# Optimization experiments

Hardware: AMD Instinct MI355X
Metric: run time of the kernel (lower is better)

## Reference

```python
import jax, jax.numpy as jnp
import numpy as np

NH = 8          # attention heads
NC = 14         # disease classes
K = 10          # aspect queries per class
E = 1024        # vision_dim == text_dim
HID = 512       # hidden_dim = vision_dim // 2
TEMP = 0.1
LN_EPS = 1e-5


def _layernorm(x, g, b):
    m = jnp.mean(x, axis=-1, keepdims=True)
    v = jnp.mean(jnp.square(x - m), axis=-1, keepdims=True)
    return (x - m) * jax.lax.rsqrt(v + LN_EPS) * g + b


def _mha(q, k, v, in_w, in_b, out_w, out_b):
    # nn.MultiheadAttention (batch_first, eval mode => dropout off)
    B, Lq, Emb = q.shape
    Lk = k.shape[1]
    dh = Emb // NH
    wq, wk, wv = jnp.split(in_w, 3, axis=0)
    bq, bk, bv = jnp.split(in_b, 3)
    qh = (q @ wq.T + bq).reshape(B, Lq, NH, dh)
    kh = (k @ wk.T + bk).reshape(B, Lk, NH, dh)
    vh = (v @ wv.T + bv).reshape(B, Lk, NH, dh)
    scale = np.float32(1.0 / np.sqrt(dh))
    scores = jnp.einsum('bqhd,bkhd->bhqk', qh, kh) * scale
    attn = jax.nn.softmax(scores, axis=-1)
    out = jnp.einsum('bhqk,bkhd->bqhd', attn, vh).reshape(B, Lq, Emb)
    out = out @ out_w.T + out_b
    return out, attn.mean(axis=1)  # avg over heads, (B, Lq, Lk)


def _l2norm(x):
    return x / jnp.maximum(jnp.linalg.norm(x, axis=-1, keepdims=True), 1e-12)


def reference(vision_features, text_embeddings, vision_global, aspect_queries,
              ch_in_w, ch_in_b, ch_out_w, ch_out_b, tp_w, tp_b,
              ca_in_w, ca_in_b, ca_out_w, ca_out_b,
              cross_ln_g, cross_ln_b, cross_fc_w, cross_fc_b,
              dir_ln_g, dir_ln_b, dir_w1, dir_b1, dir_w2, dir_b2):
    B, N, _ = vision_features.shape
    # ---- contrastive branch (1-token query / 1-token kv attention) ----
    text_proj = text_embeddings @ tp_w.T + tp_b               # (B, E)
    c_out, _ = _mha(vision_global[:, None, :], text_proj[:, None, :],
                    text_proj[:, None, :], ch_in_w, ch_in_b, ch_out_w, ch_out_b)
    sim = jnp.sum(_l2norm(c_out[:, 0, :]) * _l2norm(text_proj), axis=-1) / TEMP  # (B,)
    contrastive_logits = jnp.broadcast_to(sim[:, None], (B, NC))
    # ---- supervised branch: fused per-class cross-attention (shared K/V) ----
    q = jnp.broadcast_to(aspect_queries.reshape(1, NC * K, E), (B, NC * K, E))
    att_out, attn_w = _mha(q, vision_features, vision_features,
                           ca_in_w, ca_in_b, ca_out_w, ca_out_b)
    attended = att_out.reshape(B, NC, K, E).mean(axis=2)       # (B, NC, E)
    attention_weights = attn_w.reshape(B, NC, K, N)            # (B, NC, K, N)
    # fc_cross: LN + per-class linear row (class j feature -> class j logit)
    h = _layernorm(attended, cross_ln_g, cross_ln_b)
    logits_cross = jnp.einsum('bjd,jd->bj', h, cross_fc_w) + cross_fc_b
    # fc_direct MLP on global feature
    g = _layernorm(vision_global, dir_ln_g, dir_ln_b)
    logits_direct = jax.nn.relu(g @ dir_w1.T + dir_b1) @ dir_w2.T + dir_b2
    supervised_logits = (logits_cross + logits_direct) * 0.5
    final_logits = (supervised_logits + contrastive_logits) * 0.5
    return contrastive_logits, supervised_logits, final_logits, attention_weights


def setup_inputs() -> dict:
    key = jax.random.key(0)
    ks = jax.random.split(key, 16)
    B, N = 64, 576
    w = lambda k, s: (jax.random.normal(k, s, dtype=jnp.float32) * 0.02)
    return {
        'vision_features': jax.random.normal(ks[0], (B, N, E), dtype=jnp.float32),
        'text_embeddings': jax.random.normal(ks[1], (B, E), dtype=jnp.float32),
        'vision_global': jax.random.normal(ks[2], (B, E), dtype=jnp.float32),
        'aspect_queries': jax.random.normal(ks[3], (NC, K, E), dtype=jnp.float32) / np.sqrt(E).astype(np.float32),
        'ch_in_w': w(ks[4], (3 * E, E)), 'ch_in_b': jnp.zeros((3 * E,), jnp.float32),
        'ch_out_w': w(ks[5], (E, E)), 'ch_out_b': jnp.zeros((E,), jnp.float32),
        'tp_w': w(ks[6], (E, E)), 'tp_b': jnp.zeros((E,), jnp.float32),
        'ca_in_w': w(ks[7], (3 * E, E)), 'ca_in_b': jnp.zeros((3 * E,), jnp.float32),
        'ca_out_w': w(ks[8], (E, E)), 'ca_out_b': jnp.zeros((E,), jnp.float32),
        'cross_ln_g': jnp.ones((E,), jnp.float32), 'cross_ln_b': jnp.zeros((E,), jnp.float32),
        'cross_fc_w': w(ks[9], (NC, E)), 'cross_fc_b': jnp.zeros((NC,), jnp.float32),
        'dir_ln_g': jnp.ones((E,), jnp.float32), 'dir_ln_b': jnp.zeros((E,), jnp.float32),
        'dir_w1': w(ks[10], (HID, E)), 'dir_b1': jnp.zeros((HID,), jnp.float32),
        'dir_w2': w(ks[11], (NC, HID)), 'dir_b2': jnp.zeros((NC,), jnp.float32),
    }
```

## Files before the change

### kernel.cpp

```cpp
#include <hip/hip_runtime.h>
#include <cstdio>
#include <cstdint>

using u16 = unsigned short;
typedef __bf16 bf16x8 __attribute__((ext_vector_type(8)));
typedef float f32x4 __attribute__((ext_vector_type(4)));

#define GLOBAL_AS __attribute__((address_space(1)))
#define LDS_AS __attribute__((address_space(3)))

__device__ __forceinline__ float bf2f(u16 h) {
  return __uint_as_float(((unsigned)h) << 16);
}
__device__ __forceinline__ u16 f2bf(float f) {
  unsigned u = __float_as_uint(f);
  u += 0x7FFFu + ((u >> 16) & 1u);
  return (u16)(u >> 16);
}

__device__ __forceinline__ void async_copy16(void* lds, const void* g) {
  __builtin_amdgcn_global_load_lds((const GLOBAL_AS unsigned int*)g,
                                   (LDS_AS unsigned int*)lds, 16, 0, 0);
}

__device__ __forceinline__ float block_sum(float v, float* red) {
#pragma unroll
  for (int o = 32; o >= 1; o >>= 1) v += __shfl_xor(v, o);
  __syncthreads();
  if ((threadIdx.x & 63) == 0) red[threadIdx.x >> 6] = v;
  __syncthreads();
  return red[0] + red[1] + red[2] + red[3];
}

__global__ __launch_bounds__(256) void cvt4_kernel(
    const float* __restrict__ s0, u16* __restrict__ d0,
    const float* __restrict__ s1, u16* __restrict__ d1,
    const float* __restrict__ s2, u16* __restrict__ d2,
    const float* __restrict__ s3, u16* __restrict__ d3) {
  const float* s; u16* d; long n; long b0; long nb;
  const int b = blockIdx.x;
  if (b < 2048)      { s = s0; d = d0; n = 37748736L; b0 = b;        nb = 2048; }
  else if (b < 2816) { s = s1; d = d1; n = 3145728L;  b0 = b - 2048; nb = 768; }
  else if (b < 3072) { s = s2; d = d2; n = 1048576L;  b0 = b - 2816; nb = 256; }
  else               { s = s3; d = d3; n = 143360L;   b0 = b - 3072; nb = 35; }
  long i = (b0 * 256 + threadIdx.x) * 4;
  const long stride = nb * 1024;
  for (; i < n; i += stride) {
    float4 v = *(const float4*)(s + i);
    ushort4 o;
    o.x = f2bf(v.x); o.y = f2bf(v.y); o.z = f2bf(v.z); o.w = f2bf(v.w);
    *(ushort4*)(d + i) = o;
  }
}

template <int VTD>
__global__ __launch_bounds__(512, 2) void gemm_kvq_kernel(
    const u16* __restrict__ A, const u16* __restrict__ Bkv,
    const u16* __restrict__ Aq, const u16* __restrict__ Bq,
    u16* __restrict__ Ck, u16* __restrict__ Cvp, u16* __restrict__ Vt,
    u16* __restrict__ Cq,
    const float* __restrict__ bias, const float* __restrict__ biasq) {
  __shared__ char smem[131072];
  const int bid = blockIdx.x;
  const int t = threadIdx.x;
  const int wid = t >> 6, l = t & 63;
  const int wm = wid >> 2, wn = wid & 3;
  const int lr = l & 15, lg = l >> 4, lr7 = lr & 7;

  int mt = 0, nt = 0, qb = -1;
  const u16* Abase; const u16* Bbase; const float* bias_b;
  if (bid < 1152) {
    const int wgid = (bid & 7) * 144 + (bid >> 3);
    mt = wgid >> 3; nt = wgid & 7;
    Abase = A + (size_t)mt * 256 * 1024;
    Bbase = Bkv + (size_t)nt * 256 * 1024;
    bias_b = bias + nt * 256;
  } else {
    qb = bid - 1152;
    Abase = Aq;
    Bbase = Bq + (size_t)qb * 256 * 1024;
    bias_b = biasq + qb * 256;
  }

  const int srow = t >> 3;
  const int scx = (t & 7) ^ (srow & 7);
  const char* Asrc = (const char*)Abase + (size_t)srow * 2048 + (scx << 4);
  const char* Bsrc = (const char*)Bbase + (size_t)srow * 2048 + (scx << 4);
  const int wb = wid << 10;

  f32x4 acc[8][4] = {};

#define SA(d, r, kt) async_copy16(smem + (d)*65536 + (r)*8192 + wb, \
                                  Asrc + (size_t)(r)*131072 + (size_t)(kt)*128)
#define SB(d, r, kt) async_copy16(smem + (d)*65536 + 32768 + (r)*8192 + wb, \
                                  Bsrc + (size_t)(r)*131072 + (size_t)(kt)*128)

#define RA(d, half)                                                          \
  _Pragma("unroll")                                                          \
  for (int i = 0; i < 4; ++i) {                                              \
    const int row = wm * 128 + ((half)*4 + i) * 16 + lr;                     \
    af[i][0] = *(const bf16x8*)(smem + (d)*65536 + (row << 7) + ((lg ^ lr7) << 4));       \
    af[i][1] = *(const bf16x8*)(smem + (d)*65536 + (row << 7) + (((4 | lg) ^ lr7) << 4)); \
  }

#define RB(d, half)                                                          \
  _Pragma("unroll")                                                          \
  for (int j = 0; j < 2; ++j) {                                              \
    const int row = wn * 64 + ((half)*2 + j) * 16 + lr;                      \
    bfr[j][0] = *(const bf16x8*)(smem + (d)*65536 + 32768 + (row << 7) + ((lg ^ lr7) << 4));       \
    bfr[j][1] = *(const bf16x8*)(smem + (d)*65536 + 32768 + (row << 7) + (((4 | lg) ^ lr7) << 4)); \
  }

#define MM(mh, nh)                                                           \
  __builtin_amdgcn_s_setprio(1);                                             \
  _Pragma("unroll")                                                          \
  for (int ks = 0; ks < 2; ++ks)                                             \
    _Pragma("unroll")                                                        \
    for (int i = 0; i < 4; ++i)                                              \
      _Pragma("unroll")                                                      \
      for (int j = 0; j < 2; ++j)                                            \
        acc[(mh)*4 + i][(nh)*2 + j] = __builtin_amdgcn_mfma_f32_16x16x32_bf16( \
            af[i][ks], bfr[j][ks], acc[(mh)*4 + i][(nh)*2 + j], 0, 0, 0);    \
  __builtin_amdgcn_s_setprio(0);

  SA(0, 0, 0); SA(0, 1, 0); SA(0, 2, 0); SA(0, 3, 0);
  SB(0, 0, 0); SB(0, 1, 0); SB(0, 2, 0); SB(0, 3, 0);
  SA(1, 0, 1); SA(1, 2, 1);
  asm volatile("s_waitcnt vmcnt(2)" ::: "memory");
  __builtin_amdgcn_s_barrier();
  asm volatile("" ::: "memory");

#pragma unroll 1
  for (int kt = 0; kt < 16; ++kt) {
    const int cur = kt & 1, nxt = cur ^ 1;
    const bool pf1 = (kt < 15), pf2 = (kt < 14);
    bf16x8 af[4][2], bfr[2][2];
    RA(cur, 0);
    RB(cur, 0);
    if (pf1) { SB(nxt, 0, kt + 1); SB(nxt, 1, kt + 1); }
    __builtin_amdgcn_s_barrier();
    asm volatile("s_waitcnt lgkmcnt(0)" ::: "memory");
    MM(0, 0);
    __builtin_amdgcn_s_barrier();
    RB(cur, 1);
    if (pf1) { SB(nxt, 2, kt + 1); SB(nxt, 3, kt + 1); }
    __builtin_amdgcn_s_barrier();
    asm volatile("s_waitcnt lgkmcnt(0)" ::: "memory");
    MM(0, 1);
    if (pf1) asm volatile("s_waitcnt vmcnt(6)" ::: "memory");
    __builtin_amdgcn_s_barrier();
    RA(cur, 1);
    if (pf1) { SA(nxt, 1, kt + 1); SA(nxt, 3, kt + 1); }
    __builtin_amdgcn_s_barrier();
    asm volatile("s_waitcnt lgkmcnt(0)" ::: "memory");
    MM(1, 1);
    __builtin_amdgcn_s_barrier();
    RB(cur, 0);
    if (pf2) { SA(cur, 0, kt + 2); SA(cur, 2, kt + 2); }
    __builtin_amdgcn_s_barrier();
    asm volatile("s_waitcnt lgkmcnt(0)" ::: "memory");
    MM(1, 0);
    if (pf2)      asm volatile("s_waitcnt vmcnt(4)" ::: "memory");
    else if (pf1) asm volatile("s_waitcnt vmcnt(0)" ::: "memory");
    __builtin_amdgcn_s_barrier();
  }
#undef SA
#undef SB
#undef RA
#undef RB
#undef MM

  if (VTD && qb < 0 && nt >= 4) {
    u16* T = (u16*)smem;
    const int vc2 = t >> 1, seg = t & 1;
    const int vglob = (nt - 4) * 256 + vc2;
    const int h2 = vglob >> 7, d2 = vglob & 127;
#pragma unroll 1
    for (int mh = 0; mh < 2; ++mh) {
      __syncthreads();
      if (wm == mh) {
#pragma unroll
        for (int ni = 0; ni < 4; ++ni) {
          const int vc = wn * 64 + ni * 16 + lr;
          const float bv = bias_b[vc];
#pragma unroll
          for (int mi = 0; mi < 8; ++mi) {
            const int ml = mi * 16 + lg * 4;
            ushort4 pk;
            pk.x = f2bf(acc[mi][ni][0] + bv);
            pk.y = f2bf(acc[mi][ni][1] + bv);
            pk.z = f2bf(acc[mi][ni][2] + bv);
            pk.w = f2bf(acc[mi][ni][3] + bv);
            *(ushort4*)(T + (size_t)vc * 136 + ml) = pk;
          }
        }
      }
      __syncthreads();
      const int mg0 = mt * 256 + mh * 128 + seg * 64;
      const int bb = (unsigned)mg0 / 576u;
      const int k0 = mg0 - bb * 576;
      u16* dst = Vt + ((size_t)(bb * 8 + h2) * 128 + d2) * 576 + k0;
      const u16* src = T + (size_t)vc2 * 136 + seg * 64;
#pragma unroll
      for (int i2 = 0; i2 < 8; ++i2)
        *(uint4*)(dst + i2 * 8) = *(const uint4*)(src + i2 * 8);
    }
  } else {
    u16* D; int cb0;
    if (qb >= 0)      { D = Cq;  cb0 = qb * 256; }
    else if (nt < 4)  { D = Ck;  cb0 = nt * 256; }
    else              { D = Cvp; cb0 = (nt - 4) * 256; }
#pragma unroll
    for (int ni = 0; ni < 4; ++ni) {
      const int nc = wn * 64 + ni * 16 + lr;
      const float bv = bias_b[nc];
      const int col = cb0 + nc;
#pragma unroll
      for (int mi = 0; mi < 8; ++mi) {
#pragma unroll
        for (int rg = 0; rg < 4; ++rg) {
          const size_t m = (size_t)mt * 256 + wm * 128 + mi * 16 + lg * 4 + rg;
          D[m * 1024 + col] = f2bf(acc[mi][ni][rg] + bv);
        }
      }
    }
  }
}

template <int OUTF32>
__global__ __launch_bounds__(512, 2) void gemm_big_kernel(
    const u16* __restrict__ A, const u16* __restrict__ B, void* __restrict__ Cv,
    const float* __restrict__ bias, float scale,
    int KT, int ntx, int Mlim, int Nlim,
    long lda, long ldb, long ldc, int bdiv,
    long sA0, long sA1, long sB0, long sB1, long sC0, long sC1) {
  __shared__ u16 lds[3][24576];
  const int bid = blockIdx.x;
  const int bh = blockIdx.y;
  const int bb0 = bh / bdiv, bb1 = bh % bdiv;
  const int mt = bid / ntx, nt = bid % ntx;
  const int t = threadIdx.x;
  const int wid = t >> 6, l = t & 63;
  const int wr = wid >> 1, wc = wid & 1;
  const int lr = l & 15, lg = l >> 4, lr7 = lr & 7;

  const long ldab = lda * 2, ldbb = ldb * 2;
  const u16* Abase = A + (long)bb0 * sA0 + (long)bb1 * sA1 + (long)mt * 256 * lda;
  const u16* Bbase = B + (long)bb0 * sB0 + (long)bb1 * sB1 + (long)nt * 128 * ldb;

  const int srow = t >> 3;
  const int scx = (t & 7) ^ (srow & 7);
  const char* Asrc = (const char*)Abase + (long)srow * ldab + (scx << 4);
  const char* Bsrc = (const char*)Bbase + (long)srow * ldbb + (scx << 4);
  const int wbA = wid << 10;

  char* b0 = (char*)lds[0];
  char* b1 = (char*)lds[1];
  char* b2 = (char*)lds[2];

  f32x4 acc[4][4] = {};

#define STAGE3G(dst, kt, part)                                              \
  {                                                                         \
    const long ko = (long)(kt) * 128;                                       \
    if ((part) == 0) {                                                      \
      async_copy16((dst) + wbA,          Asrc + ko);                        \
      async_copy16((dst) + 8192 + wbA,   Asrc + 64 * ldab + ko);            \
      async_copy16((dst) + 16384 + wbA,  Asrc + 128 * ldab + ko);           \
    } else {                                                                \
      async_copy16((dst) + 24576 + wbA,  Asrc + 192 * ldab + ko);           \
      async_copy16((dst) + 32768 + wbA,  Bsrc + ko);                        \
      async_copy16((dst) + 40960 + wbA,  Bsrc + 64 * ldbb + ko);            \
    }                                                                       \
  }

#define COMPUTE_KS(p, KS)                                                   \
  {                                                                         \
    const int ccol = (((KS) << 2) | lg) ^ lr7;                              \
    const char* pA = (p) + (((wr << 6) + lr) << 7) + (ccol << 4);           \
    const char* pB = (p) + 32768 + (((wc << 6) + lr) << 7) + (ccol << 4);   \
    bf16x8 af[4], bfr[4];                                                   \
    _Pragma("unroll")                                                       \
    for (int i = 0; i < 4; ++i) {                                           \
      af[i]  = *(const bf16x8*)(pA + i * 2048);                             \
      bfr[i] = *(const bf16x8*)(pB + i * 2048);                             \
    }                                                                       \
    __builtin_amdgcn_s_setprio(1);                                          \
    _Pragma("unroll")                                                       \
    for (int mi = 0; mi < 4; ++mi)                                          \
      _Pragma("unroll")                                                     \
      for (int ni = 0; ni < 4; ++ni)                                        \
        acc[mi][ni] = __builtin_amdgcn_mfma_f32_16x16x32_bf16(              \
            af[mi], bfr[ni], acc[mi][ni], 0, 0, 0);                         \
    __builtin_amdgcn_s_setprio(0);                                          \
  }

  STAGE3G(b0, 0, 0); STAGE3G(b0, 0, 1);
  STAGE3G(b1, 1, 0); STAGE3G(b1, 1, 1);
  asm volatile("s_waitcnt vmcnt(6)" ::: "memory");
  __builtin_amdgcn_s_barrier();
  asm volatile("" ::: "memory");

  char* p0 = b0; char* p1 = b1; char* p2 = b2;
#pragma unroll 1
  for (int kt = 0; kt < KT; ++kt) {
    const bool pf = (kt < KT - 2);
    if (pf) STAGE3G(p2, kt + 2, 0);
    COMPUTE_KS(p0, 0);
    if (pf) STAGE3G(p2, kt + 2, 1);
    COMPUTE_KS(p0, 1);
    if (kt < KT - 1) {
      if (pf) asm volatile("s_waitcnt vmcnt(6)" ::: "memory");
      else    asm volatile("s_waitcnt vmcnt(0)" ::: "memory");
      __builtin_amdgcn_s_barrier();
      asm volatile("" ::: "memory");
    }
    char* tmp = p0; p0 = p1; p1 = p2; p2 = tmp;
  }
#undef STAGE3G
#undef COMPUTE_KS

  const long cBase = (long)bb0 * sC0 + (long)bb1 * sC1;
  const int mr0 = mt * 256 + wr * 64 + lg * 4;
  const int nc0 = nt * 128 + wc * 64 + lr;
#pragma unroll
  for (int ni = 0; ni < 4; ++ni) {
    const int n = nc0 + ni * 16;
    if (n >= Nlim) continue;
    const float bv = bias ? bias[n] : 0.0f;
#pragma unroll
    for (int mi = 0; mi < 4; ++mi) {
#pragma unroll
      for (int rg = 0; rg < 4; ++rg) {
        const int m = mr0 + mi * 16 + rg;
        if (m >= Mlim) continue;
        const float v = acc[mi][ni][rg] * scale + bv;
        if (OUTF32) ((float*)Cv)[cBase + (long)m * ldc + n] = v;
        else        ((u16*)Cv)[cBase + (long)m * ldc + n] = f2bf(v);
      }
    }
  }
}

__global__ __launch_bounds__(256) void transpose_v_kernel(const u16* __restrict__ V,
                                                          u16* __restrict__ Vt) {
  __shared__ u16 tile[64][65];
  const int k0 = blockIdx.x * 64;
  const int c0 = blockIdx.y * 64;
  const int b = blockIdx.z;
  const int t = threadIdx.x;
  const int tx = t & 15, ty = t >> 4;
  const u16* Vb = V + (size_t)(b * 576) * 1024;
#pragma unroll
  for (int i = 0; i < 4; ++i) {
    const int k = ty + i * 16;
    const u16* src = Vb + (size_t)(k0 + k) * 1024 + c0 + tx * 4;
    ushort2 v01 = *(const ushort2*)src;
    ushort2 v23 = *(const ushort2*)(src + 2);
    tile[k][tx * 4 + 0] = v01.x; tile[k][tx * 4 + 1] = v01.y;
    tile[k][tx * 4 + 2] = v23.x; tile[k][tx * 4 + 3] = v23.y;
  }
  __syncthreads();
  const int h = c0 >> 7, d0 = c0 & 127;
  u16* VtB = Vt + ((size_t)(b * 8 + h) * 128 + d0) * 576 + k0;
#pragma unroll
  for (int i = 0; i < 4; ++i) {
    const int d = ty + i * 16;
    u16* dst = VtB + (size_t)d * 576 + tx * 4;
    ushort2 a, bb2;
    a.x = tile[tx * 4 + 0][d]; a.y = tile[tx * 4 + 1][d];
    bb2.x = tile[tx * 4 + 2][d]; bb2.y = tile[tx * 4 + 3][d];
    *(ushort2*)dst = a; *(ushort2*)(dst + 2) = bb2;
  }
}

__global__ __launch_bounds__(512) void softmax_attn_kernel(u16* __restrict__ SP,
                                                           float* __restrict__ attnOut) {
  const int b = blockIdx.x, q = blockIdx.y;
  const int h = threadIdx.x >> 6, l = threadIdx.x & 63;
  __shared__ float pl[8][576];
  u16* row = SP + ((size_t)((b * 8 + h) * 144 + q)) * 576;
  float x[9];
#pragma unroll
  for (int i = 0; i < 9; ++i) x[i] = bf2f(row[l + 64 * i]);
  float m = x[0];
#pragma unroll
  for (int i = 1; i < 9; ++i) m = fmaxf(m, x[i]);
#pragma unroll
  for (int o = 32; o >= 1; o >>= 1) m = fmaxf(m, __shfl_xor(m, o));
  float e[9], s = 0.f;
#pragma unroll
  for (int i = 0; i < 9; ++i) { e[i] = expf(x[i] - m); s += e[i]; }
#pragma unroll
  for (int o = 32; o >= 1; o >>= 1) s += __shfl_xor(s, o);
  const float inv = 1.f / s;
#pragma unroll
  for (int i = 0; i < 9; ++i) {
    const float p = e[i] * inv;
    row[l + 64 * i] = f2bf(p);
    pl[h][l + 64 * i] = p;
  }
  __syncthreads();
  float* out = attnOut + ((size_t)(b * 140 + q)) * 576;
  for (int j = threadIdx.x; j < 576; j += 512) {
    float a = 0.f;
#pragma unroll
    for (int hh = 0; hh < 8; ++hh) a += pl[hh][j];
    out[j] = a * 0.125f;
  }
}

__global__ __launch_bounds__(256) void mean_o_kernel(const float* __restrict__ O,
                                                     u16* __restrict__ attended) {
  const int bc = blockIdx.x;
  const int b = bc / 14, c = bc % 14;
  const int t = threadIdx.x;
  const float* base = O + ((size_t)b * 140 + c * 10) * 1024;
#pragma unroll
  for (int i = 0; i < 4; ++i) {
    const int e = t + i * 256;
    float s = 0.f;
#pragma unroll
    for (int j = 0; j < 10; ++j) s += base[(size_t)j * 1024 + e];
    attended[(size_t)bc * 1024 + e] = f2bf(s * 0.1f);
  }
}

__global__ __launch_bounds__(256) void ln_crossfc_kernel(
    const float* __restrict__ ap, const float* __restrict__ g, const float* __restrict__ bb,
    const float* __restrict__ fw, const float* __restrict__ fb, float* __restrict__ out) {
  const int bc = blockIdx.x;
  const int c = bc % 14;
  const float* x = ap + (size_t)bc * 1024;
  __shared__ float red[4];
  const int t = threadIdx.x;
  float v[4];
  float s = 0.f;
#pragma unroll
  for (int i = 0; i < 4; ++i) { v[i] = x[t + i * 256]; s += v[i]; }
  const float mean = block_sum(s, red) * (1.f / 1024.f);
  float vs = 0.f;
#pragma unroll
  for (int i = 0; i < 4; ++i) { const float d = v[i] - mean; vs += d * d; }
  const float var = block_sum(vs, red) * (1.f / 1024.f);
  const float inv = rsqrtf(var + 1e-5f);
  float acc = 0.f;
#pragma unroll
  for (int i = 0; i < 4; ++i) {
    const int e = t + i * 256;
    const float h = (v[i] - mean) * inv * g[e] + bb[e];
    acc += h * fw[(size_t)c * 1024 + e];
  }
  acc = block_sum(acc, red);
  if (t == 0) out[bc] = acc + fb[c];
}

__global__ __launch_bounds__(256) void direct_mlp_kernel(
    const float* __restrict__ vg, const float* __restrict__ g, const float* __restrict__ bb,
    const float* __restrict__ w1, const float* __restrict__ b1,
    const float* __restrict__ w2, const float* __restrict__ b2, float* __restrict__ out) {
  const int b = blockIdx.x;
  __shared__ float red[4];
  __shared__ float gn[1024];
  __shared__ float h1[512];
  const int t = threadIdx.x;
  const float* x = vg + (size_t)b * 1024;
  float v[4];
  float s = 0.f;
#pragma unroll
  for (int i = 0; i < 4; ++i) { v[i] = x[t + i * 256]; s += v[i]; }
  const float mean = block_sum(s, red) * (1.f / 1024.f);
  float vs = 0.f;
#pragma unroll
  for (int i = 0; i < 4; ++i) { const float d = v[i] - mean; vs += d * d; }
  const float var = block_sum(vs, red) * (1.f / 1024.f);
  const float inv = rsqrtf(var + 1e-5f);
#pragma unroll
  for (int i = 0; i < 4; ++i) {
    const int e = t + i * 256;
    gn[e] = (v[i] - mean) * inv * g[e] + bb[e];
  }
  __syncthreads();
  for (int j = t; j < 512; j += 256) {
    float a = b1[j];
    const float4* wr = (const float4*)(w1 + (size_t)j * 1024);
    const float4* g4 = (const float4*)gn;
    for (int e = 0; e < 256; ++e) {
      float4 wv = wr[e], av = g4[e];
      a += av.x * wv.x + av.y * wv.y + av.z * wv.z + av.w * wv.w;
    }
    h1[j] = fmaxf(a, 0.f);
  }
  __syncthreads();
  for (int c = 0; c < 14; ++c) {
    float a = 0.f;
    for (int j = t; j < 512; j += 256) a += h1[j] * w2[(size_t)c * 512 + j];
    a = block_sum(a, red);
    if (t == 0) out[b * 14 + c] = a + b2[c];
  }
}

__global__ __launch_bounds__(256) void linear_f32_kernel(
    const float* __restrict__ A, const float* __restrict__ W, const float* __restrict__ bias,
    float* __restrict__ C, int N, int Kd) {
  const int r = blockIdx.x;
  const int j = blockIdx.y * 256 + threadIdx.x;
  __shared__ float a[1024];
  for (int e = threadIdx.x; e < Kd; e += 256) a[e] = A[(size_t)r * Kd + e];
  __syncthreads();
  float acc = bias ? bias[j] : 0.f;
  const float4* wr = (const float4*)(W + (size_t)j * Kd);
  const float4* a4 = (const float4*)a;
  for (int e = 0; e < Kd / 4; ++e) {
    float4 wv = wr[e], av = a4[e];
    acc += av.x * wv.x + av.y * wv.y + av.z * wv.z + av.w * wv.w;
  }
  C[(size_t)r * N + j] = acc;
}

__global__ __launch_bounds__(256) void sim_kernel(const float* __restrict__ co,
                                                  const float* __restrict__ tp,
                                                  float* __restrict__ sim) {
  const int b = blockIdx.x;
  const int t = threadIdx.x;
  __shared__ float red[4];
  const float* c = co + (size_t)b * 1024;
  const float* p = tp + (size_t)b * 1024;
  float dd = 0.f, nc = 0.f, nt = 0.f;
  for (int e = t; e < 1024; e += 256) {
    const float cv = c[e], pv = p[e];
    dd += cv * pv; nc += cv * cv; nt += pv * pv;
  }
  dd = block_sum(dd, red);
  nc = block_sum(nc, red);
  nt = block_sum(nt, red);
  if (t == 0)
    sim[b] = dd / (fmaxf(sqrtf(nc), 1e-12f) * fmaxf(sqrtf(nt), 1e-12f)) / 0.1f;
}

__global__ __launch_bounds__(256) void combine_kernel(const float* __restrict__ sim,
                                                      const float* __restrict__ lc,
                                                      const float* __restrict__ ld,
                                                      float* __restrict__ out) {
  const int i = blockIdx.x * 256 + threadIdx.x;
  if (i >= 896) return;
  const int b = i / 14;
  const float contr = sim[b];
  const float sup = 0.5f * (lc[i] + ld[i]);
  const float fin = 0.5f * (sup + contr);
  out[i] = contr;
  out[896 + i] = sup;
  out[1792 + i] = fin;
}

static constexpr size_t OFF_X    = 0;
static constexpr size_t OFF_K    = OFF_X + 75497472;
static constexpr size_t OFF_SP   = OFF_K + 75759616;
static constexpr size_t OFF_WIN  = OFF_SP + 85082112;
static constexpr size_t OFF_WOUT = OFF_WIN + 6291456;
static constexpr size_t OFF_ASP  = OFF_WOUT + 2097152;
static constexpr size_t OFF_QASP = OFF_ASP + 524288;
static constexpr size_t OFF_ATT  = OFF_QASP + 524288;
static constexpr size_t OFF_APRJ = OFF_ATT + 1835008;
static constexpr size_t OFF_TP   = OFF_APRJ + 3670016;
static constexpr size_t OFF_CV   = OFF_TP + 262144;
static constexpr size_t OFF_CO   = OFF_CV + 262144;
static constexpr size_t OFF_SIM  = OFF_CO + 262144;
static constexpr size_t OFF_LC   = OFF_SIM + 4096;
static constexpr size_t OFF_LD   = OFF_LC + 4096;
static constexpr size_t WS_SMALL = OFF_LD + 4096;
static constexpr size_t OFF_VT   = WS_SMALL;
static constexpr size_t WS_BIG   = OFF_VT + 75497472;

extern "C" void kernel_launch(void* const* d_in, const int* in_sizes, int n_in,
                              void* d_out, int out_size, void* d_ws, size_t ws_size,
                              hipStream_t stream) {
  (void)in_sizes; (void)n_in; (void)out_size;
  const float* vision_features = (const float*)d_in[0];
  const float* text_embeddings = (const float*)d_in[1];
  const float* vision_global   = (const float*)d_in[2];
  const float* aspect_queries  = (const float*)d_in[3];
  const float* ch_in_w  = (const float*)d_in[4];
  const float* ch_in_b  = (const float*)d_in[5];
  const float* ch_out_w = (const float*)d_in[6];
  const float* ch_out_b = (const float*)d_in[7];
  const float* tp_w = (const float*)d_in[8];
  const float* tp_b = (const float*)d_in[9];
  const float* ca_in_w  = (const float*)d_in[10];
  const float* ca_in_b  = (const float*)d_in[11];
  const float* ca_out_w = (const float*)d_in[12];
  const float* ca_out_b = (const float*)d_in[13];
  const float* cross_ln_g = (const float*)d_in[14];
  const float* cross_ln_b = (const float*)d_in[15];
  const float* cross_fc_w = (const float*)d_in[16];
  const float* cross_fc_b = (const float*)d_in[17];
  const float* dir_ln_g = (const float*)d_in[18];
  const float* dir_ln_b = (const float*)d_in[19];
  const float* dir_w1 = (const float*)d_in[20];
  const float* dir_b1 = (const float*)d_in[21];
  const float* dir_w2 = (const float*)d_in[22];
  const float* dir_b2 = (const float*)d_in[23];

  if (ws_size < WS_SMALL) {
    fprintf(stderr, "kernel_launch: ws too small: %zu < %zu\n", ws_size, WS_SMALL);
    return;
  }
  const bool big = (ws_size >= WS_BIG);

  char* ws = (char*)d_ws;
  u16* Xb      = (u16*)(ws + OFF_X);
  u16* Kb      = (u16*)(ws + OFF_K);
  float* O_all = (float*)(ws + OFF_K);
  u16* Vb      = (u16*)(ws + OFF_SP);
  u16* SP      = (u16*)(ws + OFF_SP);
  u16* Vt      = big ? (u16*)(ws + OFF_VT) : (u16*)(ws + OFF_X);
  u16* Win     = (u16*)(ws + OFF_WIN);
  u16* Wout    = (u16*)(ws + OFF_WOUT);
  u16* Asp     = (u16*)(ws + OFF_ASP);
  u16* Qasp    = (u16*)(ws + OFF_QASP);
  u16* Attd    = (u16*)(ws + OFF_ATT);
  float* Aprj  = (float*)(ws + OFF_APRJ);
  float* Tp    = (float*)(ws + OFF_TP);
  float* Cv2   = (float*)(ws + OFF_CV);
  float* Co    = (float*)(ws + OFF_CO);
  float* Sim   = (float*)(ws + OFF_SIM);
  float* Lc    = (float*)(ws + OFF_LC);
  float* Ld    = (float*)(ws + OFF_LD);
  float* attnOut = (float*)d_out + 2688;

  cvt4_kernel<<<3107, 256, 0, stream>>>(vision_features, Xb, ca_in_w, Win,
                                        ca_out_w, Wout, aspect_queries, Asp);

  if (big) {
    gemm_kvq_kernel<1><<<dim3(1156), 512, 0, stream>>>(
        Xb, Win + 1024 * 1024, Asp, Win, Kb, nullptr, Vt, Qasp,
        ca_in_b + 1024, ca_in_b);
  } else {
    gemm_kvq_kernel<0><<<dim3(1156), 512, 0, stream>>>(
        Xb, Win + 1024 * 1024, Asp, Win, Kb, Vb, nullptr, Qasp,
        ca_in_b + 1024, ca_in_b);
    transpose_v_kernel<<<dim3(9, 16, 64), 256, 0, stream>>>(Vb, Vt);
  }

  gemm_big_kernel<0><<<dim3(5, 512), 512, 0, stream>>>(
      Qasp, Kb, SP, nullptr, 0.08838834764831845f,
      2, 5, 140, 576, 1024, 1024, 576, 8,
      0L, 128L, 589824L, 128L, 663552L, 82944L);

  softmax_attn_kernel<<<dim3(64, 140), 512, 0, stream>>>(SP, attnOut);

  gemm_big_kernel<1><<<dim3(1, 512), 512, 0, stream>>>(
      SP, Vt, O_all, nullptr, 1.0f,
      9, 1, 140, 128, 576, 576, 1024, 8,
      663552L, 82944L, 589824L, 73728L, 143360L, 128L);

  mean_o_kernel<<<896, 256, 0, stream>>>(O_all, Attd);

  gemm_big_kernel<1><<<dim3(32, 1), 512, 0, stream>>>(
      Attd, Wout, Aprj, ca_out_b, 1.0f,
      16, 8, 896, 1024, 1024, 1024, 1024, 1,
      0L, 0L, 0L, 0L, 0L, 0L);

  ln_crossfc_kernel<<<896, 256, 0, stream>>>(Aprj, cross_ln_g, cross_ln_b,
                                             cross_fc_w, cross_fc_b, Lc);

  direct_mlp_kernel<<<64, 256, 0, stream>>>(vision_global, dir_ln_g, dir_ln_b,
                                            dir_w1, dir_b1, dir_w2, dir_b2, Ld);

  linear_f32_kernel<<<dim3(64, 4), 256, 0, stream>>>(text_embeddings, tp_w, tp_b, Tp, 1024, 1024);
  linear_f32_kernel<<<dim3(64, 4), 256, 0, stream>>>(Tp, ch_in_w + 2048 * 1024, ch_in_b + 2048, Cv2, 1024, 1024);
  linear_f32_kernel<<<dim3(64, 4), 256, 0, stream>>>(Cv2, ch_out_w, ch_out_b, Co, 1024, 1024);
  sim_kernel<<<64, 256, 0, stream>>>(Co, Tp, Sim);

  combine_kernel<<<4, 256, 0, stream>>>(Sim, Lc, Ld, (float*)d_out);
}
```

Baseline: 637.2 us.

## Average attention probabilities per class before PV to shrink the PV GEMM

```diff
diff --git a/kernel.cpp b/kernel.cpp
--- a/kernel.cpp
+++ b/kernel.cpp
@@ -374,55 +374,96 @@
   }
 }
 
-__global__ __launch_bounds__(512) void softmax_attn_kernel(u16* __restrict__ SP,
-                                                           float* __restrict__ attnOut) {
-  const int b = blockIdx.x, q = blockIdx.y;
+__global__ __launch_bounds__(512) void softmax_pm_kernel(const u16* __restrict__ SP,
+                                                         float* __restrict__ attnOut,
+                                                         u16* __restrict__ Pm) {
+  const int b = blockIdx.x, c = blockIdx.y;
   const int h = threadIdx.x >> 6, l = threadIdx.x & 63;
   __shared__ float pl[8][576];
-  u16* row = SP + ((size_t)((b * 8 + h) * 144 + q)) * 576;
-  float x[9];
-#pragma unroll
-  for (int i = 0; i < 9; ++i) x[i] = bf2f(row[l + 64 * i]);
-  float m = x[0];
-#pragma unroll
-  for (int i = 1; i < 9; ++i) m = fmaxf(m, x[i]);
-#pragma unroll
-  for (int o = 32; o >= 1; o >>= 1) m = fmaxf(m, __shfl_xor(m, o));
-  float e[9], s = 0.f;
-#pragma unroll
-  for (int i = 0; i < 9; ++i) { e[i] = expf(x[i] - m); s += e[i]; }
-#pragma unroll
-  for (int o = 32; o >= 1; o >>= 1) s += __shfl_xor(s, o);
-  const float inv = 1.f / s;
-#pragma unroll
-  for (int i = 0; i < 9; ++i) {
-    const float p = e[i] * inv;
-    row[l + 64 * i] = f2bf(p);
-    pl[h][l + 64 * i] = p;
+  float pacc[9] = {};
+#pragma unroll 1
+  for (int qq = 0; qq < 10; ++qq) {
+    const u16* row = SP + ((size_t)((b * 8 + h) * 144 + c * 10 + qq)) * 576;
+    float x[9];
+#pragma unroll
+    for (int i = 0; i < 9; ++i) x[i] = bf2f(row[l + 64 * i]);
+    float m = x[0];
+#pragma unroll
+    for (int i = 1; i < 9; ++i) m = fmaxf(m, x[i]);
+#pragma unroll
+    for (int o = 32; o >= 1; o >>= 1) m = fmaxf(m, __shfl_xor(m, o));
+    float e[9], s = 0.f;
+#pragma unroll
+    for (int i = 0; i < 9; ++i) { e[i] = expf(x[i] - m); s += e[i]; }
+#pragma unroll
+    for (int o = 32; o >= 1; o >>= 1) s += __shfl_xor(s, o);
+    const float inv = 1.f / s;
+#pragma unroll
+    for (int i = 0; i < 9; ++i) {
+      const float p = e[i] * inv;
+      pacc[i] += p;
+      pl[h][l + 64 * i] = p;
+    }
+    __syncthreads();
+    float* out = attnOut + ((size_t)(b * 140 + c * 10 + qq)) * 576;
+    {
+      const int j = threadIdx.x;
+      float a = 0.f;
+#pragma unroll
+      for (int hh = 0; hh < 8; ++hh) a += pl[hh][j];
+      out[j] = a * 0.125f;
+      if (j < 64) {
+        float a2 = 0.f;
+#pragma unroll
+        for (int hh = 0; hh < 8; ++hh) a2 += pl[hh][j + 512];
+        out[j + 512] = a2 * 0.125f;
+      }
+    }
+    __syncthreads();
+  }
+  u16* pm = Pm + ((size_t)((b * 8 + h) * 14 + c)) * 576;
+#pragma unroll
+  for (int i = 0; i < 9; ++i) pm[l + 64 * i] = f2bf(pacc[i] * 0.1f);
+}
+
+__global__ __launch_bounds__(128) void pv_small_kernel(const u16* __restrict__ Pm,
+                                                       const u16* __restrict__ Vt,
+                                                       u16* __restrict__ Attd) {
+  const int b = blockIdx.x, hq = blockIdx.y;
+  const int t = threadIdx.x;
+  const int w = t >> 6, l = t & 63;
+  const int h = hq * 2 + w;
+  const int lr = l & 15, lg = l >> 4;
+  __shared__ u16 pm[2][16][584];
+  for (int i = t; i < 2336; i += 128) {
+    const int hh = i / 1168;
+    const int rem = i - hh * 1168;
+    const int r = rem / 73, ck = rem - (rem / 73) * 73;
+    uint4 v = {0u, 0u, 0u, 0u};
+    if (r < 14 && ck < 72)
+      v = *(const uint4*)&Pm[((size_t)((b * 8 + hq * 2 + hh) * 14 + r)) * 576 + ck * 8];
+    *(uint4*)&pm[hh][r][ck * 8] = v;
   }
   __syncthreads();
-  float* out = attnOut + ((size_t)(b * 140 + q)) * 576;
-  for (int j = threadIdx.x; j < 576; j += 512) {
-    float a = 0.f;
-#pragma unroll
-    for (int hh = 0; hh < 8; ++hh) a += pl[hh][j];
-    out[j] = a * 0.125f;
-  }
-}
-
-__global__ __launch_bounds__(256) void mean_o_kernel(const float* __restrict__ O,
-                                                     u16* __restrict__ attended) {
-  const int bc = blockIdx.x;
-  const int b = bc / 14, c = bc % 14;
-  const int t = threadIdx.x;
-  const float* base = O + ((size_t)b * 140 + c * 10) * 1024;
-#pragma unroll
-  for (int i = 0; i < 4; ++i) {
-    const int e = t + i * 256;
-    float s = 0.f;
-#pragma unroll
-    for (int j = 0; j < 10; ++j) s += base[(size_t)j * 1024 + e];
-    attended[(size_t)bc * 1024 + e] = f2bf(s * 0.1f);
+  const u16* vbase = Vt + ((size_t)(b * 8 + h) * 128) * 576;
+  f32x4 acc[8] = {};
+#pragma unroll 1
+  for (int ks = 0; ks < 18; ++ks) {
+    const bf16x8 af = *(const bf16x8*)&pm[w][lr][ks * 32 + lg * 8];
+#pragma unroll
+    for (int nf = 0; nf < 8; ++nf) {
+      const bf16x8 bf = *(const bf16x8*)&vbase[(size_t)(nf * 16 + lr) * 576 + ks * 32 + lg * 8];
+      acc[nf] = __builtin_amdgcn_mfma_f32_16x16x32_bf16(af, bf, acc[nf], 0, 0, 0);
+    }
+  }
+#pragma unroll
+  for (int nf = 0; nf < 8; ++nf) {
+#pragma unroll
+    for (int rg = 0; rg < 4; ++rg) {
+      const int cc = lg * 4 + rg;
+      if (cc < 14)
+        Attd[((size_t)b * 14 + cc) * 1024 + h * 128 + nf * 16 + lr] = f2bf(acc[nf][rg]);
+    }
   }
 }
 
@@ -518,9 +559,10 @@
   C[(size_t)r * N + j] = acc;
 }
 
-__global__ __launch_bounds__(256) void sim_kernel(const float* __restrict__ co,
-                                                  const float* __restrict__ tp,
-                                                  float* __restrict__ sim) {
+__global__ __launch_bounds__(256) void sim_combine_kernel(
+    const float* __restrict__ co, const float* __restrict__ tp,
+    const float* __restrict__ lc, const float* __restrict__ ld,
+    float* __restrict__ out) {
   const int b = blockIdx.x;
   const int t = threadIdx.x;
   __shared__ float red[4];
@@ -534,23 +576,14 @@
   dd = block_sum(dd, red);
   nc = block_sum(nc, red);
   nt = block_sum(nt, red);
-  if (t == 0)
-    sim[b] = dd / (fmaxf(sqrtf(nc), 1e-12f) * fmaxf(sqrtf(nt), 1e-12f)) / 0.1f;
-}
-
-__global__ __launch_bounds__(256) void combine_kernel(const float* __restrict__ sim,
-                                                      const float* __restrict__ lc,
-                                                      const float* __restrict__ ld,
-                                                      float* __restrict__ out) {
-  const int i = blockIdx.x * 256 + threadIdx.x;
-  if (i >= 896) return;
-  const int b = i / 14;
-  const float contr = sim[b];
-  const float sup = 0.5f * (lc[i] + ld[i]);
-  const float fin = 0.5f * (sup + contr);
-  out[i] = contr;
-  out[896 + i] = sup;
-  out[1792 + i] = fin;
+  const float sim = dd / (fmaxf(sqrtf(nc), 1e-12f) * fmaxf(sqrtf(nt), 1e-12f)) / 0.1f;
+  if (t < 14) {
+    const int i = b * 14 + t;
+    const float sup = 0.5f * (lc[i] + ld[i]);
+    out[i] = sim;
+    out[896 + i] = sup;
+    out[1792 + i] = 0.5f * (sup + sim);
+  }
 }
 
 static constexpr size_t OFF_X    = 0;
@@ -610,7 +643,7 @@
   char* ws = (char*)d_ws;
   u16* Xb      = (u16*)(ws + OFF_X);
   u16* Kb      = (u16*)(ws + OFF_K);
-  float* O_all = (float*)(ws + OFF_K);
+  u16* Pm      = (u16*)(ws + OFF_K);
   u16* Vb      = (u16*)(ws + OFF_SP);
   u16* SP      = (u16*)(ws + OFF_SP);
   u16* Vt      = big ? (u16*)(ws + OFF_VT) : (u16*)(ws + OFF_X);
@@ -623,7 +656,6 @@
   float* Tp    = (float*)(ws + OFF_TP);
   float* Cv2   = (float*)(ws + OFF_CV);
   float* Co    = (float*)(ws + OFF_CO);
-  float* Sim   = (float*)(ws + OFF_SIM);
   float* Lc    = (float*)(ws + OFF_LC);
   float* Ld    = (float*)(ws + OFF_LD);
   float* attnOut = (float*)d_out + 2688;
@@ -647,14 +679,9 @@
       2, 5, 140, 576, 1024, 1024, 576, 8,
       0L, 128L, 589824L, 128L, 663552L, 82944L);
 
-  softmax_attn_kernel<<<dim3(64, 140), 512, 0, stream>>>(SP, attnOut);
-
-  gemm_big_kernel<1><<<dim3(1, 512), 512, 0, stream>>>(
-      SP, Vt, O_all, nullptr, 1.0f,
-      9, 1, 140, 128, 576, 576, 1024, 8,
-      663552L, 82944L, 589824L, 73728L, 143360L, 128L);
-
-  mean_o_kernel<<<896, 256, 0, stream>>>(O_all, Attd);
+  softmax_pm_kernel<<<dim3(64, 14), 512, 0, stream>>>(SP, attnOut, Pm);
+
+  pv_small_kernel<<<dim3(64, 4), 128, 0, stream>>>(Pm, Vt, Attd);
 
   gemm_big_kernel<1><<<dim3(32, 1), 512, 0, stream>>>(
       Attd, Wout, Aprj, ca_out_b, 1.0f,
@@ -670,7 +697,6 @@
   linear_f32_kernel<<<dim3(64, 4), 256, 0, stream>>>(text_embeddings, tp_w, tp_b, Tp, 1024, 1024);
   linear_f32_kernel<<<dim3(64, 4), 256, 0, stream>>>(Tp, ch_in_w + 2048 * 1024, ch_in_b + 2048, Cv2, 1024, 1024);
   linear_f32_kernel<<<dim3(64, 4), 256, 0, stream>>>(Cv2, ch_out_w, ch_out_b, Co, 1024, 1024);
-  sim_kernel<<<64, 256, 0, stream>>>(Co, Tp, Sim);
-
-  combine_kernel<<<4, 256, 0, stream>>>(Sim, Lc, Ld, (float*)d_out);
-}
+
+  sim_combine_kernel<<<64, 256, 0, stream>>>(Co, Tp, Lc, Ld, (float*)d_out);
+}
```

Result: faster. 603.5 us (-5.3%).
